# Optimization experiments

Hardware: AMD Instinct MI355X
Metric: run time of the kernel (lower is better)

Reference implementation:

```python
import jax, jax.numpy as jnp
import numpy as np

B, RES_IN, STRIDE, RES_OUT = 8, 64, 2, 32
C_IN, C_OUT = 256, 512
H, KD, RATIO = 8, 16, 4
VD = RATIO * KD                      # 64
KV_DIM = (RATIO + 1) * KD * H        # 640
Q_DIM = KD * H                       # 128
PROJ_IN = RATIO * KD * H             # 512
SEQ = RES_IN * RES_IN                # 4096
QLEN = RES_OUT * RES_OUT             # 1024
EPS = 1e-3                           # keras BatchNormalization default epsilon


def _bn(x, gamma, beta, mean, var):
    # inference-mode batch norm over the channel axis
    return (x - mean) * (gamma * jax.lax.rsqrt(var + EPS)) + beta


def _hard_swish(x):
    return x * jnp.clip(x + 3.0, 0.0, 6.0) * (1.0 / 6.0)


def setup_inputs() -> dict:
    key = jax.random.key(0)
    ks = jax.random.split(key, 16)
    def lin(k, fan_in, fan_out):
        return jax.random.normal(k, (fan_in, fan_out), jnp.float32) / np.sqrt(fan_in)
    def bn_params(k, c):
        k1, k2, k3 = jax.random.split(k, 3)
        gamma = 1.0 + 0.1 * jax.random.normal(k1, (c,), jnp.float32)
        beta = 0.1 * jax.random.normal(k2, (c,), jnp.float32)
        mean = 0.1 * jax.random.normal(k3, (c,), jnp.float32)
        var = jax.random.uniform(jax.random.fold_in(k, 7), (c,), jnp.float32, 0.5, 1.5)
        return gamma, beta, mean, var
    x = jax.random.normal(ks[0], (B, SEQ, C_IN), jnp.float32)
    Wkv = lin(ks[1], C_IN, KV_DIM); bkv = jnp.zeros((KV_DIM,), jnp.float32)
    g_kv, b_kv, m_kv, v_kv = bn_params(ks[2], KV_DIM)
    Wq = lin(ks[3], C_IN, Q_DIM); bq = jnp.zeros((Q_DIM,), jnp.float32)
    g_q, b_q, m_q, v_q = bn_params(ks[4], Q_DIM)
    Wp = lin(ks[5], PROJ_IN, C_OUT); bp = jnp.zeros((C_OUT,), jnp.float32)
    g_p, b_p, m_p, v_p = bn_params(ks[6], C_OUT)
    return {"x": x, "Wkv": Wkv, "bkv": bkv, "g_kv": g_kv, "b_kv": b_kv, "m_kv": m_kv, "v_kv": v_kv,
            "Wq": Wq, "bq": bq, "g_q": g_q, "b_q": b_q, "m_q": m_q, "v_q": v_q,
            "Wp": Wp, "bp": bp, "g_p": g_p, "b_p": b_p, "m_p": m_p, "v_p": v_p}


def reference(x, Wkv, bkv, g_kv, b_kv, m_kv, v_kv,
              Wq, bq, g_q, b_q, m_q, v_q,
              Wp, bp, g_p, b_p, m_p, v_p):
    scale = KD ** (-0.5)
    # keys/values: Dense + BN -> [B, SEQ, H, KD+VD]
    kv = _bn(x @ Wkv + bkv, g_kv, b_kv, m_kv, v_kv)
    kv = kv.reshape(B, SEQ, H, KD + VD)
    k = jnp.transpose(kv[..., :KD], (0, 2, 1, 3))          # [B, H, SEQ, KD]
    v = jnp.transpose(kv[..., KD:], (0, 2, 1, 3))          # [B, H, SEQ, VD]
    # strided query subsample: [B, SEQ, C] -> [B, QLEN, C]
    xq = x.reshape(B, RES_IN, RES_IN, C_IN)[:, ::STRIDE, ::STRIDE].reshape(B, QLEN, C_IN)
    q = _bn(xq @ Wq + bq, g_q, b_q, m_q, v_q)
    q = jnp.transpose(q.reshape(B, QLEN, H, KD), (0, 2, 1, 3))  # [B, H, QLEN, KD]
    attn = jnp.einsum('bhqd,bhkd->bhqk', q, k) * scale
    attn = jax.nn.softmax(attn, axis=-1)                   # [B, H, QLEN, SEQ]
    av = jnp.einsum('bhqk,bhkd->bhqd', attn, v)            # [B, H, QLEN, VD]
    # faithful to TF: transpose (0,1,3,2) then reshape to (B, -1, PROJ_IN)
    out = jnp.transpose(av, (0, 1, 3, 2)).reshape(B, -1, PROJ_IN)
    out = _bn(_hard_swish(out) @ Wp + bp, g_p, b_p, m_p, v_p)
    return out
```

## Files before the change

kernel.cpp:

```cpp
#include <hip/hip_runtime.h>

typedef __bf16 bf16_t;
typedef __bf16 bf16x4 __attribute__((ext_vector_type(4)));
typedef __bf16 bf16x8 __attribute__((ext_vector_type(8)));
typedef short s16x4 __attribute__((ext_vector_type(4)));
typedef float f32x4 __attribute__((ext_vector_type(4)));

#define BN_EPS 1e-3f

#define GLOAD_LDS16(g, l) \
  __builtin_amdgcn_global_load_lds((const __attribute__((address_space(1))) void*)(g), \
                                   (__attribute__((address_space(3))) void*)(l), 16, 0, 0)

__global__ __launch_bounds__(256) void cvt_f32_bf16(
    const float* __restrict__ in, bf16_t* __restrict__ out, long n)
{
  long i = ((long)blockIdx.x * 256 + threadIdx.x) * 8;
  if (i + 8 > n) return;
  f32x4 a = *(const f32x4*)(in + i);
  f32x4 b = *(const f32x4*)(in + i + 4);
  bf16x8 o;
  o[0] = (bf16_t)a[0]; o[1] = (bf16_t)a[1]; o[2] = (bf16_t)a[2]; o[3] = (bf16_t)a[3];
  o[4] = (bf16_t)b[0]; o[5] = (bf16_t)b[1]; o[6] = (bf16_t)b[2]; o[7] = (bf16_t)b[3];
  *(bf16x8*)(out + i) = o;
}

__global__ __launch_bounds__(256) void transpose_f32_bf16(
    const float* __restrict__ in, bf16_t* __restrict__ out, int R, int C)
{
  __shared__ bf16_t t[32][33];
  int bx = blockIdx.x * 32, by = blockIdx.y * 32;
  int tx = threadIdx.x, ty = threadIdx.y;
#pragma unroll
  for (int i = 0; i < 32; i += 8)
    t[ty + i][tx] = (bf16_t)in[(long)(by + ty + i) * C + (bx + tx)];
  __syncthreads();
#pragma unroll
  for (int i = 0; i < 32; i += 8)
    out[(long)(bx + ty + i) * R + (by + tx)] = t[tx][ty + i];
}

__global__ __launch_bounds__(256) void wkv_split_transpose(
    const float* __restrict__ in, bf16_t* __restrict__ outK, bf16_t* __restrict__ outV)
{
  __shared__ bf16_t t[32][33];
  int bx = blockIdx.x * 32, by = blockIdx.y * 32;
  int tx = threadIdx.x, ty = threadIdx.y;
#pragma unroll
  for (int i = 0; i < 32; i += 8)
    t[ty + i][tx] = (bf16_t)in[(long)(by + ty + i) * 640 + (bx + tx)];
  __syncthreads();
#pragma unroll
  for (int i = 0; i < 32; i += 8) {
    int c = bx + ty + i;
    int h = c / 80, r80 = c - h * 80;
    bf16_t v = t[tx][ty + i];
    if (r80 < 16)
      outK[(long)(h * 16 + r80) * 256 + (by + tx)] = v;
    else
      outV[(long)(h * 64 + (r80 - 16)) * 256 + (by + tx)] = v;
  }
}

__global__ __launch_bounds__(512, 1) void qkv_fused(
    const bf16_t* __restrict__ xb, const bf16_t* __restrict__ Wf,
    const float* __restrict__ bkv, const float* __restrict__ g_kv,
    const float* __restrict__ b_kv, const float* __restrict__ m_kv,
    const float* __restrict__ v_kv,
    const float* __restrict__ bq, const float* __restrict__ g_q,
    const float* __restrict__ b_q, const float* __restrict__ m_q,
    const float* __restrict__ v_q,
    bf16_t* __restrict__ Kbuf, bf16_t* __restrict__ Vtb, bf16_t* __restrict__ Qbuf)
{
  __shared__ __align__(16) char Xs[65536];
  __shared__ __align__(16) char Ws[65536];

  const int tid = threadIdx.x;
  const int lane = tid & 63, w = tid >> 6;
  const int quad = lane >> 4, l15 = lane & 15;
  const int wm = w >> 2, wn = w & 3;

  const int id = blockIdx.x;
  const int xcd = id & 7, slot = id >> 3;
  const int sd6 = slot / 6;
  const int mt = xcd * 32 + sd6;
  const int nt = slot - sd6 * 6;
  const int blockM = mt * 128, blockN = nt * 128;

  {
    const int r_lo = w * 2 + (lane >> 5);
    const int soff = ((lane & 31) ^ (r_lo & 7)) << 4;
#pragma unroll
    for (int rnd = 0; rnd < 8; rnd++) {
      const int row = rnd * 16 + r_lo;
      GLOAD_LDS16((const char*)xb + (long)(blockM + row) * 512 + soff,
                  &Xs[rnd * 8192 + w * 1024]);
      GLOAD_LDS16((const char*)Wf + (long)(blockN + row) * 512 + soff,
                  &Ws[rnd * 8192 + w * 1024]);
    }
  }
  __syncthreads();

  const int sw = l15 & 7;
  f32x4 acc[4][2] = {};
#pragma unroll
  for (int ks = 0; ks < 8; ks++) {
    const int u = ks * 4 + quad;
    const int su = (u ^ sw) << 4;
    bf16x8 af[4];
#pragma unroll
    for (int mi = 0; mi < 4; mi++)
      af[mi] = *(const bf16x8*)(&Xs[(wm * 64 + mi * 16 + l15) * 512 + su]);
    bf16x8 bf_[2];
#pragma unroll
    for (int ni = 0; ni < 2; ni++)
      bf_[ni] = *(const bf16x8*)(&Ws[(wn * 32 + ni * 16 + l15) * 512 + su]);
#pragma unroll
    for (int mi = 0; mi < 4; mi++)
#pragma unroll
      for (int ni = 0; ni < 2; ni++)
        acc[mi][ni] = __builtin_amdgcn_mfma_f32_16x16x32_bf16(af[mi], bf_[ni], acc[mi][ni], 0, 0, 0);
  }

#pragma unroll
  for (int ni = 0; ni < 2; ni++) {
    const int nfbase = blockN + wn * 32 + ni * 16;
    const int col = nfbase + l15;
    float s, t, bia;
    if (nfbase < 128) {
      int cp = (col >> 4) * 80 + (col & 15);
      s = g_kv[cp] / sqrtf(v_kv[cp] + BN_EPS);
      t = b_kv[cp] - m_kv[cp] * s;
      bia = bkv[cp];
      int h = col >> 4, d = col & 15;
#pragma unroll
      for (int mi = 0; mi < 4; mi++)
#pragma unroll
        for (int r = 0; r < 4; r++) {
          int grow = blockM + wm * 64 + mi * 16 + quad * 4 + r;
          int b = grow >> 12, seq = grow & 4095;
          float y = (acc[mi][ni][r] + bia) * s + t;
          Kbuf[((long)((b * 8 + h) * 4096 + seq)) * 16 + d] = (bf16_t)y;
        }
    } else if (nfbase < 640) {
      int ch = col - 128;
      int cp = (ch >> 6) * 80 + 16 + (ch & 63);
      s = g_kv[cp] / sqrtf(v_kv[cp] + BN_EPS);
      t = b_kv[cp] - m_kv[cp] * s;
      bia = bkv[cp];
      int h2 = ch >> 6, dv = ch & 63;
#pragma unroll
      for (int mi = 0; mi < 4; mi++)
#pragma unroll
        for (int r = 0; r < 4; r++) {
          int grow = blockM + wm * 64 + mi * 16 + quad * 4 + r;
          int b = grow >> 12, seq = grow & 4095;
          int kb = seq >> 5, s32 = seq & 31;
          int qd = (s32 & 15) >> 2, j = (s32 >> 4) * 4 + (s32 & 3);
          float y = (acc[mi][ni][r] + bia) * s + t;
          Vtb[(((long)(b * 8 + h2)) << 18) + (kb << 11) + (qd << 9) + (dv << 3) + j] = (bf16_t)y;
        }
    } else {
      int qc = col - 640;
      s = g_q[qc] / sqrtf(v_q[qc] + BN_EPS);
      t = b_q[qc] - m_q[qc] * s;
      bia = bq[qc];
      int h = qc >> 4, d = qc & 15;
#pragma unroll
      for (int mi = 0; mi < 4; mi++) {
        if ((((blockM + wm * 64 + mi * 16) >> 6) & 1) != 0) continue;
#pragma unroll
        for (int r = 0; r < 4; r += 2) {
          int grow = blockM + wm * 64 + mi * 16 + quad * 4 + r;
          int b = grow >> 12, seq = grow & 4095;
          int qp = ((seq >> 7) << 5) + ((seq & 63) >> 1);
          float y = (acc[mi][ni][r] + bia) * s + t;
          Qbuf[((long)((b * 8 + h) * 1024 + qp)) * 16 + d] = (bf16_t)(y * 0.36067376f);
        }
      }
    }
  }
}

template <int MODE>
__global__ __launch_bounds__(256, 2) void gemm_bn(
    const bf16_t* __restrict__ A, const bf16_t* __restrict__ Wt,
    const float* __restrict__ bias, const float* __restrict__ gamma,
    const float* __restrict__ beta, const float* __restrict__ mean,
    const float* __restrict__ var,
    bf16_t* __restrict__ out0, float* __restrict__ outf)
{
  constexpr int KTOT = (MODE == 2) ? 512 : 256;
  const int lane = threadIdx.x & 63;
  const int w = threadIdx.x >> 6;
  const int quad = lane >> 4, l15 = lane & 15;
  const int m0 = blockIdx.x * 64 + w * 16;
  const int n0 = blockIdx.y * 64;

  int mrow = m0 + l15;
  const bf16_t* ap = A + (long)mrow * KTOT + quad * 8;
  const bf16_t* bp = Wt + (long)(n0 + l15) * KTOT + quad * 8;

  f32x4 acc[4] = {};
#pragma unroll
  for (int kc = 0; kc < KTOT / 256; kc++) {
    bf16x8 a[8];
    bf16x8 bfr[4][8];
#pragma unroll
    for (int ks = 0; ks < 8; ks++)
      a[ks] = *(const bf16x8*)(ap + kc * 256 + ks * 32);
#pragma unroll
    for (int nt = 0; nt < 4; nt++)
#pragma unroll
      for (int ks = 0; ks < 8; ks++)
        bfr[nt][ks] = *(const bf16x8*)(bp + (long)nt * 16 * KTOT + kc * 256 + ks * 32);
#pragma unroll
    for (int ks = 0; ks < 8; ks++)
#pragma unroll
      for (int nt = 0; nt < 4; nt++)
        acc[nt] = __builtin_amdgcn_mfma_f32_16x16x32_bf16(a[ks], bfr[nt][ks], acc[nt], 0, 0, 0);
  }

#pragma unroll
  for (int nt = 0; nt < 4; nt++) {
    int col = n0 + nt * 16 + l15;
    float s = gamma[col] / sqrtf(var[col] + BN_EPS);
    float t = beta[col] - mean[col] * s;
    float bia = bias[col];
#pragma unroll
    for (int r = 0; r < 4; r++) {
      int grow = m0 + quad * 4 + r;
      float y = (acc[nt][r] + bia) * s + t;
      outf[(long)grow * 512 + col] = y;
    }
  }
}

__global__ __launch_bounds__(256, 4) void attn_kernel(
    const bf16_t* __restrict__ Q, const bf16_t* __restrict__ K,
    const bf16_t* __restrict__ Vt, bf16_t* __restrict__ outp)
{
  const int tid = threadIdx.x;
  const int lane = tid & 63, w = tid >> 6;
  const int quad = lane >> 4, l15 = lane & 15;
  const int bh = blockIdx.x & 63, qb = blockIdx.x >> 6;
  const int b = bh >> 3, h = bh & 7;
  const bf16_t* Qp = Q + (long)bh * 1024 * 16;
  const char* Kg = (const char*)(K + (long)bh * 4096 * 16);
  const char* Vg = (const char*)(Vt + ((long)bh << 18));

  __shared__ __align__(16) char Kl[4][2048];
  __shared__ __align__(16) char Vl[4][8192];

  const int q0 = qb * 64 + w * 16;
  bf16x8 qB8;
  {
    bf16x8 qv = *(const bf16x8*)(Qp + (long)(q0 + l15) * 16 + (quad & 1) * 8);
    bf16x8 zq = {};
    qB8 = (quad < 2) ? qv : zq;
  }

  f32x4 O[4] = {};
  f32x4 lpacc = {};
  const f32x4 zf = {0.f, 0.f, 0.f, 0.f};

  bf16x8 ones8;
#pragma unroll
  for (int i = 0; i < 8; i++) ones8[i] = (bf16_t)1.f;

  const char* vsrc = Vg + (long)lane * 16;
  const char* ksrc = Kg + (long)lane * 32 + (w - 2) * 16;

  auto stage = [&](int t, int buf) {
    if (w < 2) {
#pragma unroll
      for (int c = 0; c < 2; c++)
        GLOAD_LDS16(vsrc + (long)t * 8192 + (w * 2 + c) * 1024, &Vl[buf][(w * 2 + c) * 1024]);
    } else {
#pragma unroll
      for (int c = 0; c < 2; c++)
        GLOAD_LDS16(vsrc + (long)t * 8192 + ((w - 2) * 2 + 4 + c) * 1024,
                    &Vl[buf][((w - 2) * 2 + 4 + c) * 1024]);
      GLOAD_LDS16(ksrc + (long)t * 2048, &Kl[buf][(w - 2) * 1024]);
    }
  };

  const int krow_off = (quad & 1) * 1024;

  auto compute = [&](int buf) {
#pragma unroll
    for (int kh = 0; kh < 2; kh++) {
      bf16x8 k0 = *(const bf16x8*)(&Kl[buf][krow_off + (kh * 32 + l15) * 16]);
      bf16x8 k1 = *(const bf16x8*)(&Kl[buf][krow_off + (kh * 32 + 16 + l15) * 16]);
      f32x4 S0 = __builtin_amdgcn_mfma_f32_16x16x32_bf16(k0, qB8, zf, 0, 0, 0);
      f32x4 S1 = __builtin_amdgcn_mfma_f32_16x16x32_bf16(k1, qB8, zf, 0, 0, 0);
      bf16x8 pb;
      pb[0] = (bf16_t)__builtin_amdgcn_exp2f(S0[0]);
      pb[1] = (bf16_t)__builtin_amdgcn_exp2f(S0[1]);
      pb[2] = (bf16_t)__builtin_amdgcn_exp2f(S0[2]);
      pb[3] = (bf16_t)__builtin_amdgcn_exp2f(S0[3]);
      pb[4] = (bf16_t)__builtin_amdgcn_exp2f(S1[0]);
      pb[5] = (bf16_t)__builtin_amdgcn_exp2f(S1[1]);
      pb[6] = (bf16_t)__builtin_amdgcn_exp2f(S1[2]);
      pb[7] = (bf16_t)__builtin_amdgcn_exp2f(S1[3]);
      lpacc = __builtin_amdgcn_mfma_f32_16x16x32_bf16(ones8, pb, lpacc, 0, 0, 0);
#pragma unroll
      for (int dt = 0; dt < 4; dt++) {
        bf16x8 vA = *(const bf16x8*)(&Vl[buf][kh * 4096 + quad * 1024 + (dt * 16 + l15) * 16]);
        O[dt] = __builtin_amdgcn_mfma_f32_16x16x32_bf16(vA, pb, O[dt], 0, 0, 0);
      }
    }
  };

  stage(0, 0);
  stage(1, 1);
#pragma unroll 4
  for (int t = 0; t < 64; t++) {
    if (t < 63) {
      if (w < 2) asm volatile("s_waitcnt vmcnt(2)" ::: "memory");
      else       asm volatile("s_waitcnt vmcnt(3)" ::: "memory");
    } else {
      asm volatile("s_waitcnt vmcnt(0)" ::: "memory");
    }
    __builtin_amdgcn_s_barrier();
    __builtin_amdgcn_sched_barrier(0);
    if (t + 2 < 64) stage(t + 2, (t + 2) & 3);
    compute(t & 3);
  }

  float rl = __builtin_amdgcn_rcpf(lpacc[0]);
  int q = q0 + l15;
  long colq = q & 511;
  long rowbase = (long)b * 1024 + (long)h * 128 + (q >> 9);
#pragma unroll
  for (int dt = 0; dt < 4; dt++) {
#pragma unroll
    for (int r = 0; r < 4; r++) {
      int dv = dt * 16 + quad * 4 + r;
      float val = O[dt][r] * rl;
      float hs = val * fminf(fmaxf(val + 3.f, 0.f), 6.f) * (1.f / 6.f);
      outp[(rowbase + (long)dv * 2) * 512 + colq] = (bf16_t)hs;
    }
  }
}

extern "C" void kernel_launch(void* const* d_in, const int* in_sizes, int n_in,
                              void* d_out, int out_size, void* d_ws, size_t ws_size,
                              hipStream_t stream)
{
  const float* x    = (const float*)d_in[0];
  const float* Wkv  = (const float*)d_in[1];
  const float* bkv  = (const float*)d_in[2];
  const float* g_kv = (const float*)d_in[3];
  const float* b_kv = (const float*)d_in[4];
  const float* m_kv = (const float*)d_in[5];
  const float* v_kv = (const float*)d_in[6];
  const float* Wq   = (const float*)d_in[7];
  const float* bq   = (const float*)d_in[8];
  const float* g_q  = (const float*)d_in[9];
  const float* b_q  = (const float*)d_in[10];
  const float* m_q  = (const float*)d_in[11];
  const float* v_q  = (const float*)d_in[12];
  const float* Wp   = (const float*)d_in[13];
  const float* bp   = (const float*)d_in[14];
  const float* g_p  = (const float*)d_in[15];
  const float* b_p  = (const float*)d_in[16];
  const float* m_p  = (const float*)d_in[17];
  const float* v_p  = (const float*)d_in[18];

  char* ws = (char*)d_ws;
  bf16_t* xb   = (bf16_t*)ws; ws += (long)8 * 4096 * 256 * 2;
  bf16_t* WkT  = (bf16_t*)ws; ws += (long)128 * 256 * 2;
  bf16_t* WvT  = (bf16_t*)ws; ws += (long)512 * 256 * 2;
  bf16_t* Wq_t = (bf16_t*)ws; ws += (long)128 * 256 * 2;
  bf16_t* Wp_t = (bf16_t*)ws; ws += (long)512 * 512 * 2;
  bf16_t* Qbuf = (bf16_t*)ws; ws += (long)64 * 1024 * 16 * 2;
  bf16_t* Kbuf = (bf16_t*)ws; ws += (long)64 * 4096 * 16 * 2;
  bf16_t* Vtb  = (bf16_t*)ws; ws += (long)64 * 64 * 4096 * 2;
  bf16_t* outp = (bf16_t*)ws; ws += (long)8192 * 512 * 2;
  ws += 16384;

  cvt_f32_bf16<<<dim3(4096), 256, 0, stream>>>(x, xb, (long)8 * 4096 * 256);

  wkv_split_transpose<<<dim3(20, 8), dim3(32, 8), 0, stream>>>(Wkv, WkT, WvT);
  transpose_f32_bf16<<<dim3(4, 8),   dim3(32, 8), 0, stream>>>(Wq, Wq_t, 256, 128);
  transpose_f32_bf16<<<dim3(16, 16), dim3(32, 8), 0, stream>>>(Wp, Wp_t, 512, 512);

  qkv_fused<<<dim3(1536), 512, 0, stream>>>(xb, WkT,
      bkv, g_kv, b_kv, m_kv, v_kv, bq, g_q, b_q, m_q, v_q,
      Kbuf, Vtb, Qbuf);

  attn_kernel<<<dim3(1024), 256, 0, stream>>>(Qbuf, Kbuf, Vtb, outp);

  gemm_bn<2><<<dim3(128, 8), 256, 0, stream>>>(outp, Wp_t, bp, g_p, b_p, m_p, v_p, nullptr, (float*)d_out);
}
```

Baseline: 239.2 us.

## Tile projection GEMM through LDS and deepen attention K/V prefetch

Replaces the register-only projection GEMM, which loaded A and W fragments straight from global memory, with a 128x128-tiled kernel. That kernel stages A and W in XOR-swizzled LDS using direct global-to-LDS loads and maps blocks to XCDs so neighbouring tiles share L2. It also moves the attention kernel's K/V pipeline from 2-ahead to 3-ahead staging using the 4-slot ring, with adjusted vmcnt waits. Both changes aim to cut global-memory latency and redundant loads. The cost is more LDS per block (128KB, one block per CU) and more in-flight loads.

```diff
diff --git a/kernel.cpp b/kernel.cpp
--- a/kernel.cpp
+++ b/kernel.cpp
@@ -182,57 +182,78 @@
   }
 }
 
-template <int MODE>
-__global__ __launch_bounds__(256, 2) void gemm_bn(
+__global__ __launch_bounds__(512, 1) void proj_fused(
     const bf16_t* __restrict__ A, const bf16_t* __restrict__ Wt,
     const float* __restrict__ bias, const float* __restrict__ gamma,
     const float* __restrict__ beta, const float* __restrict__ mean,
-    const float* __restrict__ var,
-    bf16_t* __restrict__ out0, float* __restrict__ outf)
-{
-  constexpr int KTOT = (MODE == 2) ? 512 : 256;
-  const int lane = threadIdx.x & 63;
-  const int w = threadIdx.x >> 6;
+    const float* __restrict__ var, float* __restrict__ outf)
+{
+  __shared__ __align__(16) char Xs[65536];
+  __shared__ __align__(16) char Wl[65536];
+
+  const int tid = threadIdx.x;
+  const int lane = tid & 63, w = tid >> 6;
   const int quad = lane >> 4, l15 = lane & 15;
-  const int m0 = blockIdx.x * 64 + w * 16;
-  const int n0 = blockIdx.y * 64;
-
-  int mrow = m0 + l15;
-  const bf16_t* ap = A + (long)mrow * KTOT + quad * 8;
-  const bf16_t* bp = Wt + (long)(n0 + l15) * KTOT + quad * 8;
-
-  f32x4 acc[4] = {};
-#pragma unroll
-  for (int kc = 0; kc < KTOT / 256; kc++) {
-    bf16x8 a[8];
-    bf16x8 bfr[4][8];
-#pragma unroll
-    for (int ks = 0; ks < 8; ks++)
-      a[ks] = *(const bf16x8*)(ap + kc * 256 + ks * 32);
-#pragma unroll
-    for (int nt = 0; nt < 4; nt++)
-#pragma unroll
-      for (int ks = 0; ks < 8; ks++)
-        bfr[nt][ks] = *(const bf16x8*)(bp + (long)nt * 16 * KTOT + kc * 256 + ks * 32);
-#pragma unroll
-    for (int ks = 0; ks < 8; ks++)
-#pragma unroll
-      for (int nt = 0; nt < 4; nt++)
-        acc[nt] = __builtin_amdgcn_mfma_f32_16x16x32_bf16(a[ks], bfr[nt][ks], acc[nt], 0, 0, 0);
-  }
-
-#pragma unroll
-  for (int nt = 0; nt < 4; nt++) {
-    int col = n0 + nt * 16 + l15;
+  const int wm = w >> 2, wn = w & 3;
+
+  const int id = blockIdx.x;
+  const int xcd = id & 7, slot = id >> 3;
+  const int mt = xcd * 8 + (slot >> 2);
+  const int nt = slot & 3;
+  const int blockM = mt * 128, blockN = nt * 128;
+
+  const int r_lo = w * 2 + (lane >> 5);
+  const int soff = ((lane & 31) ^ (r_lo & 7)) << 4;
+  const int sw = l15 & 7;
+  f32x4 acc[4][2] = {};
+
+#pragma unroll
+  for (int kc = 0; kc < 2; kc++) {
+    if (kc) __syncthreads();
+#pragma unroll
+    for (int rnd = 0; rnd < 8; rnd++) {
+      const int row = rnd * 16 + r_lo;
+      GLOAD_LDS16((const char*)A  + (long)(blockM + row) * 1024 + kc * 512 + soff,
+                  &Xs[rnd * 8192 + w * 1024]);
+      GLOAD_LDS16((const char*)Wt + (long)(blockN + row) * 1024 + kc * 512 + soff,
+                  &Wl[rnd * 8192 + w * 1024]);
+    }
+    __syncthreads();
+
+#pragma unroll
+    for (int ks = 0; ks < 8; ks++) {
+      const int u = ks * 4 + quad;
+      const int su = (u ^ sw) << 4;
+      bf16x8 af[4];
+#pragma unroll
+      for (int mi = 0; mi < 4; mi++)
+        af[mi] = *(const bf16x8*)(&Xs[(wm * 64 + mi * 16 + l15) * 512 + su]);
+      bf16x8 bw[2];
+#pragma unroll
+      for (int ni = 0; ni < 2; ni++)
+        bw[ni] = *(const bf16x8*)(&Wl[(wn * 32 + ni * 16 + l15) * 512 + su]);
+#pragma unroll
+      for (int mi = 0; mi < 4; mi++)
+#pragma unroll
+        for (int ni = 0; ni < 2; ni++)
+          acc[mi][ni] = __builtin_amdgcn_mfma_f32_16x16x32_bf16(af[mi], bw[ni], acc[mi][ni], 0, 0, 0);
+    }
+  }
+
+#pragma unroll
+  for (int ni = 0; ni < 2; ni++) {
+    int col = blockN + wn * 32 + ni * 16 + l15;
     float s = gamma[col] / sqrtf(var[col] + BN_EPS);
     float t = beta[col] - mean[col] * s;
     float bia = bias[col];
 #pragma unroll
-    for (int r = 0; r < 4; r++) {
-      int grow = m0 + quad * 4 + r;
-      float y = (acc[nt][r] + bia) * s + t;
-      outf[(long)grow * 512 + col] = y;
-    }
+    for (int mi = 0; mi < 4; mi++)
+#pragma unroll
+      for (int r = 0; r < 4; r++) {
+        int grow = blockM + wm * 64 + mi * 16 + quad * 4 + r;
+        float y = (acc[mi][ni][r] + bia) * s + t;
+        outf[(long)grow * 512 + col] = y;
+      }
   }
 }
 
@@ -314,9 +335,13 @@
 
   stage(0, 0);
   stage(1, 1);
+  stage(2, 2);
 #pragma unroll 4
   for (int t = 0; t < 64; t++) {
-    if (t < 63) {
+    if (t + 2 < 64) {
+      if (w < 2) asm volatile("s_waitcnt vmcnt(4)" ::: "memory");
+      else       asm volatile("s_waitcnt vmcnt(6)" ::: "memory");
+    } else if (t + 1 < 64) {
       if (w < 2) asm volatile("s_waitcnt vmcnt(2)" ::: "memory");
       else       asm volatile("s_waitcnt vmcnt(3)" ::: "memory");
     } else {
@@ -324,7 +349,7 @@
     }
     __builtin_amdgcn_s_barrier();
     __builtin_amdgcn_sched_barrier(0);
-    if (t + 2 < 64) stage(t + 2, (t + 2) & 3);
+    if (t + 3 < 64) stage(t + 3, (t + 3) & 3);
     compute(t & 3);
   }
 
@@ -392,5 +417,5 @@
 
   attn_kernel<<<dim3(1024), 256, 0, stream>>>(Qbuf, Kbuf, Vtb, outp);
 
-  gemm_bn<2><<<dim3(128, 8), 256, 0, stream>>>(outp, Wp_t, bp, g_p, b_p, m_p, v_p, nullptr, (float*)d_out);
-}
+  proj_fused<<<dim3(256), 512, 0, stream>>>(outp, Wp_t, bp, g_p, b_p, m_p, v_p, (float*)d_out);
+}
```

New measurement: 213.7 us. 10.7% less time.
